# Optimization experiments

Hardware: AMD Instinct MI355X
Metric: run time of the kernel (lower is better)

## Reference

```python
import jax, jax.numpy as jnp
import numpy as np

EMBEDDING_DIM = 64
N_EMBEDDINGS = 512


def setup_inputs() -> dict:
    key = jax.random.key(0)
    k1, k2 = jax.random.split(key)
    inputs = jax.random.normal(k1, (32, 64, 64, 64), dtype=jnp.float32)  # NCHW, C==embedding_dim
    weight = jax.random.normal(k2, (N_EMBEDDINGS, EMBEDDING_DIM), dtype=jnp.float32)
    return {"inputs": inputs, "weight": weight}


def reference(inputs, weight):
    # NCHW -> NHWC, flatten to [N, D]
    x = jnp.transpose(inputs, (0, 2, 3, 1))  # [B, H, W, D]
    in_shape = x.shape
    flat = x.reshape(-1, EMBEDDING_DIM)  # [N, D]

    distances = (
        jnp.sum(flat * flat, axis=1, keepdims=True)
        + jnp.sum(weight * weight, axis=1)
        - 2.0 * flat @ weight.T
    )
    idx = jnp.argmin(distances, axis=1)  # [N]

    # one-hot @ weight is just a gather
    quantized = weight[idx].reshape(in_shape)  # [B, H, W, D]

    # commitment loss: mse(stop_grad(quantized), x)
    e_latent_loss = jnp.mean(jnp.square(jax.lax.stop_gradient(quantized) - x))

    # straight-through estimator
    quantized = x + jax.lax.stop_gradient(quantized - x)

    return jnp.transpose(quantized, (0, 3, 1, 2)), e_latent_loss
```

## Files before the change

### kernel.cpp

```cpp
#include <hip/hip_runtime.h>
#include <math.h>

typedef short bf16x8 __attribute__((ext_vector_type(8)));
typedef float f32x4 __attribute__((ext_vector_type(4)));

#define VQ_D 64
#define VQ_K 512
#define VQ_NQ 131072
#define VQ_TOTAL 8388608
#define NT 32
#define NCK 8
#define TAU 8e-3f

typedef __attribute__((address_space(1))) void as1_void;
typedef __attribute__((address_space(3))) void as3_void;

__device__ __forceinline__ void gll16(const void* g, void* l) {
    __builtin_amdgcn_global_load_lds((as1_void*)(void*)g, (as3_void*)l, 16, 0, 0);
}
__device__ __forceinline__ void gll4(const void* g, void* l) {
    __builtin_amdgcn_global_load_lds((as1_void*)(void*)g, (as3_void*)l, 4, 0, 0);
}

__device__ __forceinline__ ushort bf16_rne(float f) {
    uint u = __builtin_bit_cast(uint, f);
    u += 0x7fffu + ((u >> 16) & 1u);
    return (ushort)(u >> 16);
}
__device__ __forceinline__ float bf16_to_f(ushort h) {
    uint u = ((uint)h) << 16;
    return __builtin_bit_cast(float, u);
}

__global__ __launch_bounds__(128) void vq_prep(const float* __restrict__ w,
                                               ushort* __restrict__ wfrag,
                                               float* __restrict__ wn,
                                               float* __restrict__ out) {
    if (blockIdx.x == 0 && threadIdx.x == 0) out[VQ_TOTAL] = 0.f;
    const int tid = threadIdx.x;
    const int k = (blockIdx.x << 4) + (tid >> 3);
    const int g = tid & 7;
    const float4* row = (const float4*)(w + k * VQ_D);
    float4 a = row[2 * g], b4 = row[2 * g + 1];
    float v[8] = {a.x, a.y, a.z, a.w, b4.x, b4.y, b4.z, b4.w};
    ushort hi[8], lo[8];
    float nrm = 0.f;
#pragma unroll
    for (int j = 0; j < 8; ++j) {
        nrm = fmaf(v[j], v[j], nrm);
        hi[j] = bf16_rne(v[j]);
        lo[j] = bf16_rne(v[j] - bf16_to_f(hi[j]));
    }
    nrm += __shfl_xor(nrm, 1, 64);
    nrm += __shfl_xor(nrm, 2, 64);
    nrm += __shfl_xor(nrm, 4, 64);
    if (g == 0) wn[k] = nrm;
    const int t = k >> 4, col = k & 15;
    const int quad = g & 3, fh = g >> 2;
    bf16x8* basez = (bf16x8*)wfrag + t * 256 + quad * 16 + col;
    basez[fh * 64]       = *(bf16x8*)hi;
    basez[(2 + fh) * 64] = *(bf16x8*)lo;
}

__global__ __launch_bounds__(512, 8) void vq_main(const float* __restrict__ in,
                                                  const float* __restrict__ w,
                                                  const ushort* __restrict__ wfrag,
                                                  const float* __restrict__ wng,
                                                  float* __restrict__ out) {
    __shared__ __align__(16) char bstage[2][16384];
    __shared__ float wn_lds[VQ_K];
    __shared__ float xn_lds[128];
    __shared__ float best_lds[128], sec_lds[128];
    __shared__ int   bi_lds[128], si_lds[128];
    __shared__ double loss_lds[8];

    const int tid  = threadIdx.x;
    const int lane = tid & 63;
    const int wid  = tid >> 6;
    const int col  = lane & 15;
    const int quad = lane >> 4;
    const int n0  = blockIdx.x * 128;
    const int b   = n0 >> 12;
    const int hw0 = n0 & 4095;
    const float* xg0 = in + (b << 18) + hw0;

    {
        const char* gs = (const char*)wfrag + tid * 16;
        char* lb = &bstage[0][0] + wid * 1024;
        gll16(gs, lb);
        gll16(gs + 8192, lb + 8192);
        gll4(wng + tid, (char*)wn_lds + wid * 256);
    }

    bf16x8 ah0, ah1, al0, al1;
    {
        const float* xq = xg0 + wid * 16 + col;
        float sx = 0.f;
        ushort h0[8], l0[8], h1[8], l1[8];
#pragma unroll
        for (int j = 0; j < 8; ++j) {
            float v0 = xq[(quad * 8 + j) << 12];
            float v1 = xq[(32 + quad * 8 + j) << 12];
            sx = fmaf(v0, v0, sx);
            sx = fmaf(v1, v1, sx);
            h0[j] = bf16_rne(v0); l0[j] = bf16_rne(v0 - bf16_to_f(h0[j]));
            h1[j] = bf16_rne(v1); l1[j] = bf16_rne(v1 - bf16_to_f(h1[j]));
        }
        ah0 = *(bf16x8*)h0; al0 = *(bf16x8*)l0;
        ah1 = *(bf16x8*)h1; al1 = *(bf16x8*)l1;
        sx += __shfl_xor(sx, 16, 64);
        sx += __shfl_xor(sx, 32, 64);
        if (quad == 0) xn_lds[wid * 16 + col] = sx;
    }

    __syncthreads();

    float best[4], sec[4];
#pragma unroll
    for (int r = 0; r < 4; ++r) { best[r] = 3.0e38f; sec[r] = 3.0e38f; }

#pragma unroll 1
    for (int c = 0; c < NCK; ++c) {
        char* const bcur = &bstage[c & 1][0];
        if (c + 1 < NCK) {
            const char* gs = (const char*)wfrag + (c + 1) * 16384 + tid * 16;
            char* lb = &bstage[(c + 1) & 1][0] + wid * 1024;
            gll16(gs, lb);
            gll16(gs + 8192, lb + 8192);
        }
#pragma unroll
        for (int s = 0; s < 4; ++s) {
            const int t2 = 4 * c + s;
            const char* rb = bcur + s * 4096 + lane * 16;
            bf16x8 bh0 = *(const bf16x8*)(rb);
            bf16x8 bh1 = *(const bf16x8*)(rb + 1024);
            bf16x8 bl0 = *(const bf16x8*)(rb + 2048);
            bf16x8 bl1 = *(const bf16x8*)(rb + 3072);
            const float wnv = wn_lds[t2 * 16 + col];
            f32x4 accP = {0.f, 0.f, 0.f, 0.f}, accQ = {0.f, 0.f, 0.f, 0.f};
            __builtin_amdgcn_s_setprio(1);
            accP = __builtin_amdgcn_mfma_f32_16x16x32_bf16(ah0, bh0, accP, 0, 0, 0);
            accP = __builtin_amdgcn_mfma_f32_16x16x32_bf16(ah1, bh1, accP, 0, 0, 0);
            accQ = __builtin_amdgcn_mfma_f32_16x16x32_bf16(ah0, bl0, accQ, 0, 0, 0);
            accQ = __builtin_amdgcn_mfma_f32_16x16x32_bf16(ah1, bl1, accQ, 0, 0, 0);
            accQ = __builtin_amdgcn_mfma_f32_16x16x32_bf16(al0, bh0, accQ, 0, 0, 0);
            accQ = __builtin_amdgcn_mfma_f32_16x16x32_bf16(al1, bh1, accQ, 0, 0, 0);
            __builtin_amdgcn_s_setprio(0);
#pragma unroll
            for (int j = 0; j < 4; ++j) {
                float dist = fmaf(-2.f, accP[j] + accQ[j], wnv);
                uint u = (__builtin_bit_cast(uint, dist) & 0xFFFFFFE0u) | (uint)t2;
                float key = __builtin_bit_cast(float, u);
                float m = fmaxf(best[j], key);
                best[j] = fminf(best[j], key);
                sec[j]  = fminf(sec[j], m);
            }
        }
        __syncthreads();
    }

    float bD[4], sD[4];
    int bI[4], sI[4];
#pragma unroll
    for (int r = 0; r < 4; ++r) {
        uint ub = __builtin_bit_cast(uint, best[r]);
        uint us = __builtin_bit_cast(uint, sec[r]);
        bI[r] = (int)(ub & 31u) * 16 + col;
        sI[r] = (int)(us & 31u) * 16 + col;
        bD[r] = __builtin_bit_cast(float, ub & 0xFFFFFFE0u);
        sD[r] = __builtin_bit_cast(float, us & 0xFFFFFFE0u);
    }

#pragma unroll
    for (int off = 1; off < 16; off <<= 1) {
#pragma unroll
        for (int r = 0; r < 4; ++r) {
            float ob = __shfl_xor(bD[r], off, 64);
            float os = __shfl_xor(sD[r], off, 64);
            int   oi = __shfl_xor(bI[r], off, 64);
            int   oc = __shfl_xor(sI[r], off, 64);
            bool oWins = (ob < bD[r]) || (ob == bD[r] && oi < bI[r]);
            float nb  = oWins ? ob    : bD[r];
            int   ni  = oWins ? oi    : bI[r];
            float c1  = oWins ? bD[r] : ob;
            int   ci1 = oWins ? bI[r] : oi;
            float c2  = oWins ? os    : sD[r];
            int   ci2 = oWins ? oc    : sI[r];
            bool c1w = (c1 < c2) || (c1 == c2 && ci1 < ci2);
            sD[r] = c1w ? c1  : c2;
            sI[r] = c1w ? ci1 : ci2;
            bD[r] = nb; bI[r] = ni;
        }
    }
    if (col == 0) {
#pragma unroll
        for (int r = 0; r < 4; ++r) {
            const int q = wid * 16 + quad * 4 + r;
            best_lds[q] = bD[r]; sec_lds[q] = sD[r];
            bi_lds[q] = bI[r];   si_lds[q] = sI[r];
        }
    }
    __syncthreads();

    {
        const int q = tid >> 2, part = tid & 3;
        float cb = best_lds[q], cs = sec_lds[q];
        int cbi = bi_lds[q], csi = si_lds[q];
        double chosen = (double)cb;
        if (cs - cb < TAU) {
            const float* wb  = w + cbi * VQ_D + part * 16;
            const float* ws2 = w + csi * VQ_D + part * 16;
            const float* xqp = xg0 + q;
            double nb = 0.0, dotb = 0.0, ns = 0.0, dots = 0.0;
#pragma unroll
            for (int d0 = 0; d0 < 16; ++d0) {
                const int d = part * 16 + d0;
                double xv = (double)xqp[d << 12];
                double wbv = (double)wb[d0], wsv = (double)ws2[d0];
                nb = fma(wbv, wbv, nb); dotb = fma(xv, wbv, dotb);
                ns = fma(wsv, wsv, ns); dots = fma(xv, wsv, dots);
            }
#pragma unroll
            for (int off = 1; off < 4; off <<= 1) {
                nb   += __shfl_xor(nb,   off, 64);
                dotb += __shfl_xor(dotb, off, 64);
                ns   += __shfl_xor(ns,   off, 64);
                dots += __shfl_xor(dots, off, 64);
            }
            double db = nb - 2.0 * dotb, ds = ns - 2.0 * dots;
            if (ds < db || (ds == db && csi < cbi)) { cbi = csi; chosen = ds; }
            else                                    { chosen = db; }
        }
        if (part == 0) bi_lds[q] = cbi;
        double lq = (part == 0) ? ((double)xn_lds[q] + chosen) : 0.0;
#pragma unroll
        for (int off = 32; off > 0; off >>= 1)
            lq += __shfl_down(lq, off, 64);
        if (lane == 0) loss_lds[wid] = lq;
    }
    __syncthreads();
    if (tid == 0) {
        double s = 0.0;
#pragma unroll
        for (int wv = 0; wv < 8; ++wv) s += loss_lds[wv];
        atomicAdd(out + VQ_TOTAL, (float)(s * (1.0 / (double)VQ_TOTAL)));
    }

    {
        const int q = tid & 127, quarter = tid >> 7;
        const float4* wrow = (const float4*)(w + bi_lds[q] * VQ_D) + quarter * 4;
        float* op = out + (b << 18) + hw0 + q;
#pragma unroll
        for (int u = 0; u < 4; ++u) {
            float4 v = wrow[u];
            const int d = quarter * 16 + 4 * u;
            op[(d + 0) << 12] = v.x;
            op[(d + 1) << 12] = v.y;
            op[(d + 2) << 12] = v.z;
            op[(d + 3) << 12] = v.w;
        }
    }
}

extern "C" void kernel_launch(void* const* d_in, const int* in_sizes, int n_in,
                              void* d_out, int out_size, void* d_ws, size_t ws_size,
                              hipStream_t stream) {
    const float* in = (const float*)d_in[0];
    const float* w  = (const float*)d_in[1];
    float* out = (float*)d_out;

    ushort* wfrag = (ushort*)d_ws;
    float*  wn    = (float*)((char*)d_ws + 131072);

    vq_prep<<<32, 128, 0, stream>>>(w, wfrag, wn, out);
    vq_main<<<VQ_NQ / 128, 512, 0, stream>>>(in, w, wfrag, wn, out);
}
```

Measured before the change: 116.7 us.

## Deepen codebook staging to 4-buffer ring with per-block phase-staggered chunks

Splits the codebook fragment stream into 16 chunks of 8 KB and stages them through a four-slot LDS ring, keeping up to three loads in flight. Explicit vmcnt waits plus a single barrier per chunk replace the old end-of-iteration __syncthreads. Each block also starts at a different chunk, set by blockIdx mod 16, so concurrent blocks read different parts of the codebook. This is meant to hide global-to-LDS latency and spread L2 traffic. The cost is twice as many loop iterations and reliance on hand-counted waitcnt ordering, which also has to cover the earlier input loads.

```diff
diff --git a/kernel.cpp b/kernel.cpp
--- a/kernel.cpp
+++ b/kernel.cpp
@@ -8,8 +8,7 @@
 #define VQ_K 512
 #define VQ_NQ 131072
 #define VQ_TOTAL 8388608
-#define NT 32
-#define NCK 8
+#define NCH 16
 #define TAU 8e-3f
 
 typedef __attribute__((address_space(1))) void as1_void;
@@ -67,7 +66,7 @@
                                                   const ushort* __restrict__ wfrag,
                                                   const float* __restrict__ wng,
                                                   float* __restrict__ out) {
-    __shared__ __align__(16) char bstage[2][16384];
+    __shared__ __align__(16) char bstage[4][8192];
     __shared__ float wn_lds[VQ_K];
     __shared__ float xn_lds[128];
     __shared__ float best_lds[128], sec_lds[128];
@@ -83,12 +82,12 @@
     const int b   = n0 >> 12;
     const int hw0 = n0 & 4095;
     const float* xg0 = in + (b << 18) + hw0;
-
-    {
-        const char* gs = (const char*)wfrag + tid * 16;
-        char* lb = &bstage[0][0] + wid * 1024;
-        gll16(gs, lb);
-        gll16(gs + 8192, lb + 8192);
+    const int phase = blockIdx.x & 15;
+
+    const char* wf = (const char*)wfrag;
+
+    {
+        gll16(wf + phase * 8192 + tid * 16, &bstage[0][0] + wid * 1024);
         gll4(wng + tid, (char*)wn_lds + wid * 256);
     }
 
@@ -113,24 +112,31 @@
         if (quad == 0) xn_lds[wid * 16 + col] = sx;
     }
 
-    __syncthreads();
+    {
+        const int cc1 = (phase + 1) & 15, cc2 = (phase + 2) & 15;
+        gll16(wf + cc1 * 8192 + tid * 16, &bstage[1][0] + wid * 1024);
+        gll16(wf + cc2 * 8192 + tid * 16, &bstage[2][0] + wid * 1024);
+    }
 
     float best[4], sec[4];
 #pragma unroll
     for (int r = 0; r < 4; ++r) { best[r] = 3.0e38f; sec[r] = 3.0e38f; }
 
 #pragma unroll 1
-    for (int c = 0; c < NCK; ++c) {
-        char* const bcur = &bstage[c & 1][0];
-        if (c + 1 < NCK) {
-            const char* gs = (const char*)wfrag + (c + 1) * 16384 + tid * 16;
-            char* lb = &bstage[(c + 1) & 1][0] + wid * 1024;
-            gll16(gs, lb);
-            gll16(gs + 8192, lb + 8192);
-        }
-#pragma unroll
-        for (int s = 0; s < 4; ++s) {
-            const int t2 = 4 * c + s;
+    for (int c = 0; c < NCH; ++c) {
+        if (c < NCH - 2)      asm volatile("s_waitcnt vmcnt(2)" ::: "memory");
+        else if (c == NCH - 2) asm volatile("s_waitcnt vmcnt(1)" ::: "memory");
+        else                  asm volatile("s_waitcnt vmcnt(0)" ::: "memory");
+        __builtin_amdgcn_s_barrier();
+        if (c + 3 < NCH) {
+            const int cn = (c + 3 + phase) & 15;
+            gll16(wf + cn * 8192 + tid * 16, &bstage[(c + 3) & 3][0] + wid * 1024);
+        }
+        const int cc = (c + phase) & 15;
+        const char* bcur = &bstage[c & 3][0];
+#pragma unroll
+        for (int s = 0; s < 2; ++s) {
+            const int t2 = 2 * cc + s;
             const char* rb = bcur + s * 4096 + lane * 16;
             bf16x8 bh0 = *(const bf16x8*)(rb);
             bf16x8 bh1 = *(const bf16x8*)(rb + 1024);
@@ -156,7 +162,6 @@
                 sec[j]  = fminf(sec[j], m);
             }
         }
-        __syncthreads();
     }
 
     float bD[4], sD[4];
```

After: 119.4 us. +2.3%, slower.
